# Optimization experiments

Measured on AMD Instinct MI355X. Metric: run time of the kernel, lower is better.

Reference implementation:

```python
import jax, jax.numpy as jnp
import numpy as np

N = 100000  # nodes
E = 500000  # directed edges (before self-loops)

def _glorot(key, fi, fo):
    s = np.sqrt(6.0 / (fi + fo)).astype(np.float32)
    return jax.random.uniform(key, (fi, fo), jnp.float32, -s, s)

def setup_inputs() -> dict:
    key = jax.random.key(0)
    ks = jax.random.split(key, 6)
    x = jax.random.normal(ks[0], (N, 128), jnp.float32)
    edge_index = jax.random.randint(ks[1], (2, E), 0, N, dtype=jnp.int64)
    return {
        "x": x,
        "edge_index": edge_index,
        "W1": _glorot(ks[2], 128, 512), "b1": jnp.zeros((512,), jnp.float32),
        "W2": _glorot(ks[3], 512, 768), "b2": jnp.zeros((768,), jnp.float32),
        "W3": _glorot(ks[4], 768, 512), "b3": jnp.zeros((512,), jnp.float32),
        "W4": _glorot(ks[5], 512, 128), "b4": jnp.zeros((128,), jnp.float32),
    }

def reference(x, edge_index, W1, b1, W2, b2, W3, b3, W4, b4):
    # PyG GCNConv: add self-loops, deg from dst index, sym-normalized scatter-add.
    loops = jnp.arange(N, dtype=edge_index.dtype)
    src = jnp.concatenate([edge_index[0], loops])  # [E+N]
    dst = jnp.concatenate([edge_index[1], loops])  # [E+N]
    deg = jax.ops.segment_sum(jnp.ones_like(dst, jnp.float32), dst, num_segments=N)
    dinv = jax.lax.rsqrt(deg)  # deg >= 1 thanks to self-loops
    norm = (dinv[src] * dinv[dst])[:, None]  # [E+N, 1]

    def gcn_conv(h, W, b):
        hw = h @ W                                  # [N, Fout] dense linear
        msg = norm * hw[src]                        # [E+N, Fout] gather + scale
        return jax.ops.segment_sum(msg, dst, num_segments=N) + b

    h = jax.nn.gelu(gcn_conv(x, W1, b1), approximate=False)
    h = jax.nn.gelu(gcn_conv(h, W2, b2), approximate=False)
    h = jax.nn.gelu(gcn_conv(h, W3, b3), approximate=False)
    return gcn_conv(h, W4, b4)
```

## Files before the change

kernel.cpp:

```cpp
#include <hip/hip_runtime.h>

typedef short bf16x8 __attribute__((ext_vector_type(8)));
typedef float f32x4 __attribute__((ext_vector_type(4)));

__device__ __forceinline__ float b2f(unsigned short u) {
  union { unsigned int i; float f; } x; x.i = ((unsigned int)u) << 16; return x.f;
}
__device__ __forceinline__ unsigned short f2b(float f) {
  union { float f; unsigned int u; } x; x.f = f;
  unsigned int r = (x.u + 0x7FFFu + ((x.u >> 16) & 1u)) >> 16;
  return (unsigned short)r;
}
__device__ __forceinline__ float gelu_f(float v) {
  return 0.5f * v * (1.0f + erff(v * 0.70710678118654752440f));
}


__global__ void count_kernel(const int* __restrict__ ei, int E, int* __restrict__ cnt) {
  int e = blockIdx.x * 256 + threadIdx.x;
  if (e < E) atomicAdd(&cnt[ei[E + e]], 1);
}

__global__ void dinv_kernel(const int* __restrict__ cnt, float* __restrict__ dinv, int Nn) {
  int n = blockIdx.x * 256 + threadIdx.x;
  if (n < Nn) dinv[n] = rsqrtf((float)cnt[n] + 1.0f);
}


__global__ __launch_bounds__(256) void scanA_kernel(const int* __restrict__ cnt,
                                                    int* __restrict__ bsum, int Nn) {
  __shared__ int red[256];
  const int t = threadIdx.x;
  const int base = blockIdx.x * 512 + t * 2;
  int a = (base < Nn) ? cnt[base] : 0;
  int b = (base + 1 < Nn) ? cnt[base + 1] : 0;
  red[t] = a + b;
  __syncthreads();
  for (int d = 128; d > 0; d >>= 1) {
    if (t < d) red[t] += red[t + d];
    __syncthreads();
  }
  if (t == 0) bsum[blockIdx.x] = red[0];
}

__global__ __launch_bounds__(256) void scanB_kernel(const int* __restrict__ bsum,
                                                    int* __restrict__ boff,
                                                    int* __restrict__ rowstart,
                                                    int NBLK, int Nn) {
  __shared__ int sh[256];
  const int t = threadIdx.x;
  sh[t] = (t < NBLK) ? bsum[t] : 0;
  __syncthreads();
  for (int d = 1; d < 256; d <<= 1) {
    int x = sh[t];
    int add = (t >= d) ? sh[t - d] : 0;
    __syncthreads();
    sh[t] = x + add;
    __syncthreads();
  }
  if (t < NBLK) boff[t] = (t == 0) ? 0 : sh[t - 1];
  if (t == NBLK - 1) rowstart[Nn] = sh[t];
}

__global__ __launch_bounds__(256) void scanC_kernel(const int* __restrict__ cnt,
                                                    const int* __restrict__ boff,
                                                    int* __restrict__ rowstart,
                                                    int* __restrict__ cursor, int Nn) {
  __shared__ int sh[256];
  const int t = threadIdx.x;
  const int base = blockIdx.x * 512 + t * 2;
  int a = (base < Nn) ? cnt[base] : 0;
  int b = (base + 1 < Nn) ? cnt[base + 1] : 0;
  sh[t] = a + b;
  __syncthreads();
  for (int d = 1; d < 256; d <<= 1) {
    int x = sh[t];
    int add = (t >= d) ? sh[t - d] : 0;
    __syncthreads();
    sh[t] = x + add;
    __syncthreads();
  }
  const int off = boff[blockIdx.x] + ((t == 0) ? 0 : sh[t - 1]);
  if (base < Nn) { rowstart[base] = off; cursor[base] = off; }
  if (base + 1 < Nn) { rowstart[base + 1] = off + a; cursor[base + 1] = off + a; }
}

__global__ void fill_kernel(const int* __restrict__ ei, int E, const float* __restrict__ dinv,
                            int* __restrict__ cursor, int* __restrict__ ssrc,
                            float* __restrict__ snorm) {
  int e = blockIdx.x * 256 + threadIdx.x;
  if (e < E) {
    int s = ei[e], d = ei[E + e];
    int pos = atomicAdd(&cursor[d], 1);
    ssrc[pos] = s;
    snorm[pos] = dinv[s] * dinv[d];
  }
}

__global__ void wtrans_kernel(const float* __restrict__ W, unsigned short* __restrict__ WT,
                              int K, int N) {
  int i = blockIdx.x * 256 + threadIdx.x;
  if (i < K * N) {
    int n = i / K, k = i - n * K;
    WT[i] = f2b(W[k * N + n]);
  }
}


template <int F, bool INF32, bool OUTF32, bool HASBIAS, bool DOGELU>
__global__ __launch_bounds__(256) void agg_kernel(
    const int* __restrict__ rowstart, const int* __restrict__ ssrc,
    const float* __restrict__ snorm, const float* __restrict__ dinv,
    const void* __restrict__ inv, const float* __restrict__ bias,
    void* __restrict__ outv, int Nn) {
  constexpr int V = F / 64;
  const int lane = threadIdx.x & 63;
  const int node = blockIdx.x * 4 + (threadIdx.x >> 6);
  if (node >= Nn) return;
  const int base = lane * V;
  float acc[V];
  {
    float w = dinv[node]; w = w * w;
    if constexpr (INF32) {
      const float* in = (const float*)inv + (size_t)node * F + base;
      if constexpr (V == 2) {
        float2 v = *(const float2*)in; acc[0] = w * v.x; acc[1] = w * v.y;
      } else {
        float4 v0 = *(const float4*)in; float4 v1 = *(const float4*)(in + 4);
        acc[0] = w * v0.x; acc[1] = w * v0.y; acc[2] = w * v0.z; acc[3] = w * v0.w;
        acc[4] = w * v1.x; acc[5] = w * v1.y; acc[6] = w * v1.z; acc[7] = w * v1.w;
      }
    } else {
      const unsigned short* in = (const unsigned short*)inv + (size_t)node * F + base;
      if constexpr (V == 2) {
        unsigned int v = *(const unsigned int*)in;
        acc[0] = w * b2f(v & 0xffffu); acc[1] = w * b2f(v >> 16);
      } else {
        bf16x8 v = *(const bf16x8*)in;
#pragma unroll
        for (int i = 0; i < 8; ++i) acc[i] = w * b2f((unsigned short)v[i]);
      }
    }
  }
  const int e0 = rowstart[node], e1 = rowstart[node + 1];
  for (int e = e0; e < e1; ++e) {
    const int s = ssrc[e];
    const float w = snorm[e];
    if constexpr (INF32) {
      const float* in = (const float*)inv + (size_t)s * F + base;
      if constexpr (V == 2) {
        float2 v = *(const float2*)in; acc[0] += w * v.x; acc[1] += w * v.y;
      } else {
        float4 v0 = *(const float4*)in; float4 v1 = *(const float4*)(in + 4);
        acc[0] += w * v0.x; acc[1] += w * v0.y; acc[2] += w * v0.z; acc[3] += w * v0.w;
        acc[4] += w * v1.x; acc[5] += w * v1.y; acc[6] += w * v1.z; acc[7] += w * v1.w;
      }
    } else {
      const unsigned short* in = (const unsigned short*)inv + (size_t)s * F + base;
      if constexpr (V == 2) {
        unsigned int v = *(const unsigned int*)in;
        acc[0] += w * b2f(v & 0xffffu); acc[1] += w * b2f(v >> 16);
      } else {
        bf16x8 v = *(const bf16x8*)in;
#pragma unroll
        for (int i = 0; i < 8; ++i) acc[i] += w * b2f((unsigned short)v[i]);
      }
    }
  }
  if constexpr (HASBIAS) {
#pragma unroll
    for (int i = 0; i < V; ++i) acc[i] += bias[base + i];
  }
  if constexpr (DOGELU) {
#pragma unroll
    for (int i = 0; i < V; ++i) acc[i] = gelu_f(acc[i]);
  }
  if constexpr (OUTF32) {
    float* out = (float*)outv + (size_t)node * F + base;
#pragma unroll
    for (int i = 0; i < V; ++i) out[i] = acc[i];
  } else {
    unsigned short* out = (unsigned short*)outv + (size_t)node * F + base;
    if constexpr (V == 2) {
      unsigned int pack = (unsigned int)f2b(acc[0]) | ((unsigned int)f2b(acc[1]) << 16);
      *(unsigned int*)out = pack;
    } else {
      bf16x8 o;
#pragma unroll
      for (int i = 0; i < 8; ++i) o[i] = (short)f2b(acc[i]);
      *(bf16x8*)out = o;
    }
  }
}


template <bool HASBIAS, bool DOGELU>
__global__ __launch_bounds__(512, 2) void gemm256(
    const unsigned short* __restrict__ A, const unsigned short* __restrict__ BT,
    const float* __restrict__ bias, unsigned short* __restrict__ C,
    int N, int K, int NT) {
  __shared__ alignas(16) unsigned short As[2][256 * 64];
  __shared__ alignas(16) unsigned short Bs[2][256 * 64];
  const int tid = threadIdx.x;
  const int lane = tid & 63;
  const int wid = tid >> 6;
  const int wr = wid >> 2;
  const int wc = wid & 3;
  const int rr = lane & 15, rg = lane >> 4;

  const int G = gridDim.x;
  const int q = G >> 3, r = G & 7;
  const int xcd = blockIdx.x & 7, ii = blockIdx.x >> 3;
  const int w = (xcd < r ? xcd * (q + 1) : r * (q + 1) + (xcd - r) * q) + ii;
  const int bx = w / NT;
  const int by = w - bx * NT;
  const size_t brow = (size_t)bx * 256;
  const size_t bcol = (size_t)by * 256;

  const int nt = K >> 6;

  auto stage = [&](int t) {
    const int kb = t << 6;
    const int buf = t & 1;
#pragma unroll
    for (int j = 0; j < 4; ++j) {
      const int s = tid + 512 * j;
      const int row = s >> 3;
      const int lslot = (s & 7) ^ (row & 7);
      const unsigned short* gA = A + (brow + row) * K + kb + lslot * 8;
      __builtin_amdgcn_global_load_lds((const __attribute__((address_space(1))) void*)gA,
          (__attribute__((address_space(3))) void*)(&As[buf][s * 8]), 16, 0, 0);
      const unsigned short* gB = BT + (bcol + row) * K + kb + lslot * 8;
      __builtin_amdgcn_global_load_lds((const __attribute__((address_space(1))) void*)gB,
          (__attribute__((address_space(3))) void*)(&Bs[buf][s * 8]), 16, 0, 0);
    }
  };

  f32x4 acc[8][4] = {};
  stage(0);
  __syncthreads();
  for (int t = 0; t < nt; ++t) {
    if (t + 1 < nt) stage(t + 1);
    const int buf = t & 1;
    bf16x8 bq[2][4];
#pragma unroll
    for (int kk = 0; kk < 2; ++kk)
#pragma unroll
      for (int nb = 0; nb < 4; ++nb) {
        const int R = wc * 64 + nb * 16 + rr;
        const int ps = (kk * 4 + rg) ^ (R & 7);
        bq[kk][nb] = *(const bf16x8*)(&Bs[buf][R * 64 + ps * 8]);
      }
#pragma unroll
    for (int mb = 0; mb < 8; ++mb) {
      const int R = wr * 128 + mb * 16 + rr;
      const int ps0 = rg ^ (R & 7);
      const int ps1 = (4 + rg) ^ (R & 7);
      bf16x8 a0 = *(const bf16x8*)(&As[buf][R * 64 + ps0 * 8]);
      bf16x8 a1 = *(const bf16x8*)(&As[buf][R * 64 + ps1 * 8]);
#pragma unroll
      for (int nb = 0; nb < 4; ++nb)
        acc[mb][nb] = __builtin_amdgcn_mfma_f32_16x16x32_bf16(a0, bq[0][nb], acc[mb][nb], 0, 0, 0);
#pragma unroll
      for (int nb = 0; nb < 4; ++nb)
        acc[mb][nb] = __builtin_amdgcn_mfma_f32_16x16x32_bf16(a1, bq[1][nb], acc[mb][nb], 0, 0, 0);
    }
    __syncthreads();
  }
#pragma unroll
  for (int mb = 0; mb < 8; ++mb) {
    size_t row0 = brow + wr * 128 + mb * 16 + rg * 4;
#pragma unroll
    for (int nb = 0; nb < 4; ++nb) {
      size_t col = bcol + wc * 64 + nb * 16 + rr;
      float bv = 0.0f;
      if constexpr (HASBIAS) bv = bias[col];
#pragma unroll
      for (int r2 = 0; r2 < 4; ++r2) {
        float v = acc[mb][nb][r2] + bv;
        if constexpr (DOGELU) v = gelu_f(v);
        C[(row0 + r2) * N + col] = f2b(v);
      }
    }
  }
}


template <bool HASBIAS, bool DOGELU>
__global__ __launch_bounds__(256) void gemm_bt(
    const unsigned short* __restrict__ A, const unsigned short* __restrict__ BT,
    const float* __restrict__ bias, unsigned short* __restrict__ C,
    int N, int K, int NT) {
  __shared__ alignas(16) unsigned short Asl[128 * 32];
  __shared__ alignas(16) unsigned short Bsl[128 * 32];
  const int tid = threadIdx.x;
  const int lane = tid & 63;
  const int wid = tid >> 6;

  const int G = gridDim.x;
  const int q = G >> 3, r = G & 7;
  const int xcd = blockIdx.x & 7, ii = blockIdx.x >> 3;
  const int w = (xcd < r ? xcd * (q + 1) : r * (q + 1) + (xcd - r) * q) + ii;
  const int bx = w / NT;
  const int by = w - bx * NT;

  const size_t brow = (size_t)bx * 128;
  const size_t bcol = (size_t)by * 128;
  const int wr = (wid >> 1) * 64;
  const int wc = (wid & 1) * 64;
  const int rr = lane & 15, rg = lane >> 4;
  f32x4 acc[4][4] = {};
  const int KT = K >> 5;
  for (int kt = 0; kt < KT; ++kt) {
    const int kb = kt << 5;
#pragma unroll
    for (int rsub = 0; rsub < 2; ++rsub) {
      const int c = tid + rsub * 256;
      const int arow = c >> 2;
      const int jlog = (c & 3) ^ ((arow >> 1) & 3);
      const unsigned short* gA = A + (brow + arow) * K + kb + jlog * 8;
      __builtin_amdgcn_global_load_lds((const __attribute__((address_space(1))) void*)gA,
                                       (__attribute__((address_space(3))) void*)(&Asl[c * 8]),
                                       16, 0, 0);
      const unsigned short* gB = BT + (bcol + arow) * K + kb + jlog * 8;
      __builtin_amdgcn_global_load_lds((const __attribute__((address_space(1))) void*)gB,
                                       (__attribute__((address_space(3))) void*)(&Bsl[c * 8]),
                                       16, 0, 0);
    }
    __syncthreads();
    bf16x8 af[4], bfr[4];
#pragma unroll
    for (int m = 0; m < 4; ++m) {
      const int R = wr + m * 16 + rr;
      af[m] = *(const bf16x8*)(&Asl[R * 32 + ((rg ^ ((R >> 1) & 3)) * 8)]);
    }
#pragma unroll
    for (int n = 0; n < 4; ++n) {
      const int R = wc + n * 16 + rr;
      bfr[n] = *(const bf16x8*)(&Bsl[R * 32 + ((rg ^ ((R >> 1) & 3)) * 8)]);
    }
#pragma unroll
    for (int m = 0; m < 4; ++m)
#pragma unroll
      for (int n = 0; n < 4; ++n)
        acc[m][n] = __builtin_amdgcn_mfma_f32_16x16x32_bf16(af[m], bfr[n], acc[m][n], 0, 0, 0);
    __syncthreads();
  }
#pragma unroll
  for (int m = 0; m < 4; ++m) {
    size_t row0 = brow + wr + m * 16 + rg * 4;
#pragma unroll
    for (int n = 0; n < 4; ++n) {
      size_t col = bcol + wc + n * 16 + rr;
      float bv = 0.0f;
      if constexpr (HASBIAS) bv = bias[col];
#pragma unroll
      for (int r2 = 0; r2 < 4; ++r2) {
        float v = acc[m][n][r2] + bv;
        if constexpr (DOGELU) v = gelu_f(v);
        C[(row0 + r2) * N + col] = f2b(v);
      }
    }
  }
}


extern "C" void kernel_launch(void* const* d_in, const int* in_sizes, int n_in,
                              void* d_out, int out_size, void* d_ws, size_t ws_size,
                              hipStream_t stream) {
  const float* x = (const float*)d_in[0];
  const int* ei = (const int*)d_in[1];
  const float* W1 = (const float*)d_in[2]; const float* b1 = (const float*)d_in[3];
  const float* W2 = (const float*)d_in[4]; const float* b2 = (const float*)d_in[5];
  const float* W3 = (const float*)d_in[6]; const float* b3 = (const float*)d_in[7];
  const float* W4 = (const float*)d_in[8]; const float* b4 = (const float*)d_in[9];

  const int Nn = in_sizes[0] / 128;
  const int E = in_sizes[1] / 2;
  const int Mpad = (Nn + 255) & ~255;

  char* p = (char*)d_ws;
  auto alloc = [&](size_t bytes) {
    char* r = p;
    p += (bytes + 255) & ~(size_t)255;
    return r;
  };
  float* dinv = (float*)alloc((size_t)Nn * 4);
  int* cnt = (int*)alloc((size_t)Nn * 4);
  int* rowstart = (int*)alloc((size_t)(Nn + 1) * 4);
  int* cursor = (int*)alloc((size_t)Nn * 4);
  int* ssrc = (int*)alloc((size_t)E * 4);
  float* snorm = (float*)alloc((size_t)E * 4);
  int* bsum = (int*)alloc((size_t)256 * 4);
  int* boff = (int*)alloc((size_t)256 * 4);
  unsigned short* WT1 = (unsigned short*)alloc((size_t)512 * 128 * 2);
  unsigned short* WT2 = (unsigned short*)alloc((size_t)768 * 512 * 2);
  unsigned short* WT3 = (unsigned short*)alloc((size_t)512 * 768 * 2);
  unsigned short* WT4 = (unsigned short*)alloc((size_t)128 * 512 * 2);
  unsigned short* bufA = (unsigned short*)alloc((size_t)Mpad * 512 * 2);
  unsigned short* bufB = (unsigned short*)alloc((size_t)Mpad * 768 * 2);

  const int EB = (E + 255) / 256;
  const int NB = (Nn + 255) / 256;
  const int AGGB = (Nn + 3) / 4;
  const int MT128 = Mpad / 128;
  const int MT256 = Mpad / 256;
  const int NSCAN = (Nn + 511) / 512;

  hipMemsetAsync(cnt, 0, (size_t)Nn * 4, stream);
  count_kernel<<<EB, 256, 0, stream>>>(ei, E, cnt);
  dinv_kernel<<<NB, 256, 0, stream>>>(cnt, dinv, Nn);
  scanA_kernel<<<NSCAN, 256, 0, stream>>>(cnt, bsum, Nn);
  scanB_kernel<<<1, 256, 0, stream>>>(bsum, boff, rowstart, NSCAN, Nn);
  scanC_kernel<<<NSCAN, 256, 0, stream>>>(cnt, boff, rowstart, cursor, Nn);
  fill_kernel<<<EB, 256, 0, stream>>>(ei, E, dinv, cursor, ssrc, snorm);
  wtrans_kernel<<<(128 * 512 + 255) / 256, 256, 0, stream>>>(W1, WT1, 128, 512);
  wtrans_kernel<<<(512 * 768 + 255) / 256, 256, 0, stream>>>(W2, WT2, 512, 768);
  wtrans_kernel<<<(768 * 512 + 255) / 256, 256, 0, stream>>>(W3, WT3, 768, 512);
  wtrans_kernel<<<(512 * 128 + 255) / 256, 256, 0, stream>>>(W4, WT4, 512, 128);

  agg_kernel<128, true, false, false, false><<<AGGB, 256, 0, stream>>>(
      rowstart, ssrc, snorm, dinv, x, nullptr, bufA, Nn);
  gemm256<true, true><<<MT256 * 2, 512, 0, stream>>>(bufA, WT1, b1, bufB, 512, 128, 2);

  agg_kernel<512, false, false, false, false><<<AGGB, 256, 0, stream>>>(
      rowstart, ssrc, snorm, dinv, bufB, nullptr, bufA, Nn);
  gemm256<true, true><<<MT256 * 3, 512, 0, stream>>>(bufA, WT2, b2, bufB, 768, 512, 3);

  gemm256<false, false><<<MT256 * 2, 512, 0, stream>>>(bufB, WT3, nullptr, bufA, 512, 768, 2);
  agg_kernel<512, false, false, true, true><<<AGGB, 256, 0, stream>>>(
      rowstart, ssrc, snorm, dinv, bufA, b3, bufB, Nn);

  gemm_bt<false, false><<<MT128 * 1, 256, 0, stream>>>(bufB, WT4, nullptr, bufA, 128, 512, 1);
  agg_kernel<128, false, true, true, false><<<AGGB, 256, 0, stream>>>(
      rowstart, ssrc, snorm, dinv, bufA, b4, d_out, Nn);
}
```

Baseline: 767.5 us.

## Deepen GEMM LDS pipeline to 4 buffers with K=32 slices and explicit vmcnt waits

Splits each 256x256 GEMM tile's K loop into 32-wide slices held in a 4-deep LDS ring, prefetching two slices ahead. The full __syncthreads is replaced by explicit s_waitcnt vmcnt plus s_barrier, so the next loads stay in flight while the current slice is computed. The LDS swizzle is adapted to the 32-wide rows, and s_setprio is raised around the MFMA block. The cost is twice as many barriers per K, and hand-counted vmcnt values that must match the number of loads issued per stage.

```diff
diff --git a/kernel.cpp b/kernel.cpp
--- a/kernel.cpp
+++ b/kernel.cpp
@@ -199,8 +199,8 @@
     const unsigned short* __restrict__ A, const unsigned short* __restrict__ BT,
     const float* __restrict__ bias, unsigned short* __restrict__ C,
     int N, int K, int NT) {
-  __shared__ alignas(16) unsigned short As[2][256 * 64];
-  __shared__ alignas(16) unsigned short Bs[2][256 * 64];
+  __shared__ alignas(16) unsigned short As[4][256 * 32];
+  __shared__ alignas(16) unsigned short Bs[4][256 * 32];
   const int tid = threadIdx.x;
   const int lane = tid & 63;
   const int wid = tid >> 6;
@@ -217,16 +217,16 @@
   const size_t brow = (size_t)bx * 256;
   const size_t bcol = (size_t)by * 256;
 
-  const int nt = K >> 6;
+  const int nt = K >> 5;
 
   auto stage = [&](int t) {
-    const int kb = t << 6;
-    const int buf = t & 1;
-#pragma unroll
-    for (int j = 0; j < 4; ++j) {
+    const int kb = t << 5;
+    const int buf = t & 3;
+#pragma unroll
+    for (int j = 0; j < 2; ++j) {
       const int s = tid + 512 * j;
-      const int row = s >> 3;
-      const int lslot = (s & 7) ^ (row & 7);
+      const int row = s >> 2;
+      const int lslot = (s & 3) ^ ((row >> 1) & 3);
       const unsigned short* gA = A + (brow + row) * K + kb + lslot * 8;
       __builtin_amdgcn_global_load_lds((const __attribute__((address_space(1))) void*)gA,
           (__attribute__((address_space(3))) void*)(&As[buf][s * 8]), 16, 0, 0);
@@ -238,34 +238,41 @@
 
   f32x4 acc[8][4] = {};
   stage(0);
-  __syncthreads();
+  stage(1);
+  asm volatile("s_waitcnt vmcnt(4)" ::: "memory");
+  __builtin_amdgcn_s_barrier();
+  __builtin_amdgcn_sched_barrier(0);
+
   for (int t = 0; t < nt; ++t) {
-    if (t + 1 < nt) stage(t + 1);
-    const int buf = t & 1;
-    bf16x8 bq[2][4];
-#pragma unroll
-    for (int kk = 0; kk < 2; ++kk)
-#pragma unroll
-      for (int nb = 0; nb < 4; ++nb) {
-        const int R = wc * 64 + nb * 16 + rr;
-        const int ps = (kk * 4 + rg) ^ (R & 7);
-        bq[kk][nb] = *(const bf16x8*)(&Bs[buf][R * 64 + ps * 8]);
-      }
+    const int buf = t & 3;
+    if (t + 2 < nt) stage(t + 2);
+    bf16x8 bq[4];
+#pragma unroll
+    for (int nb = 0; nb < 4; ++nb) {
+      const int R = wc * 64 + nb * 16 + rr;
+      const int ps = rg ^ ((R >> 1) & 3);
+      bq[nb] = *(const bf16x8*)(&Bs[buf][R * 32 + ps * 8]);
+    }
+    __builtin_amdgcn_s_setprio(1);
 #pragma unroll
     for (int mb = 0; mb < 8; ++mb) {
       const int R = wr * 128 + mb * 16 + rr;
-      const int ps0 = rg ^ (R & 7);
-      const int ps1 = (4 + rg) ^ (R & 7);
-      bf16x8 a0 = *(const bf16x8*)(&As[buf][R * 64 + ps0 * 8]);
-      bf16x8 a1 = *(const bf16x8*)(&As[buf][R * 64 + ps1 * 8]);
+      const int ps = rg ^ ((R >> 1) & 3);
+      bf16x8 a = *(const bf16x8*)(&As[buf][R * 32 + ps * 8]);
 #pragma unroll
       for (int nb = 0; nb < 4; ++nb)
-        acc[mb][nb] = __builtin_amdgcn_mfma_f32_16x16x32_bf16(a0, bq[0][nb], acc[mb][nb], 0, 0, 0);
-#pragma unroll
-      for (int nb = 0; nb < 4; ++nb)
-        acc[mb][nb] = __builtin_amdgcn_mfma_f32_16x16x32_bf16(a1, bq[1][nb], acc[mb][nb], 0, 0, 0);
-    }
-    __syncthreads();
+        acc[mb][nb] = __builtin_amdgcn_mfma_f32_16x16x32_bf16(a, bq[nb], acc[mb][nb], 0, 0, 0);
+    }
+    __builtin_amdgcn_s_setprio(0);
+    if (t + 1 < nt) {
+      __builtin_amdgcn_sched_barrier(0);
+      if (t + 2 < nt)
+        asm volatile("s_waitcnt vmcnt(4)" ::: "memory");
+      else
+        asm volatile("s_waitcnt vmcnt(0)" ::: "memory");
+      __builtin_amdgcn_s_barrier();
+      __builtin_amdgcn_sched_barrier(0);
+    }
   }
 #pragma unroll
   for (int mb = 0; mb < 8; ++mb) {
```

Result: slower. 818.4 us (+6.6%).
